# Kernel tuning notes

Measured on AMD Instinct MI355X. Metric: run time of the kernel, lower is better.

The kernel has to match this reference:

```python
import jax, jax.numpy as jnp
import numpy as np


def setup_inputs() -> dict:
    key = jax.random.key(0)
    ks = jax.random.split(key, 6)
    m, d, n, p = 4096, 1024, 16, 1024  # tokens, input_dim, num_experts, output_dim (=slots)
    h = (d + p) * 2 // 3  # 1365, hidden_dim per original module
    s = 0.02
    return {
        "x": jax.random.normal(ks[0], (m, d), jnp.float32),
        "phi": jax.random.normal(ks[1], (d, n, p), jnp.float32) * s,
        "W1": jax.random.normal(ks[2], (n, d, h), jnp.float32) * s,
        "b1": jax.random.normal(ks[3], (n, h), jnp.float32) * s,
        "W2": jax.random.normal(ks[4], (n, h, p), jnp.float32) * s,
        "b2": jax.random.normal(ks[5], (n, p), jnp.float32) * s,
    }


def reference(x, phi, W1, b1, W2, b2):
    # logits: [m, n, p] = tokens x experts x slots
    logits = jnp.einsum('md,dnp->mnp', x, phi)
    # Dispatch weights: softmax over tokens' expert axis (dim=1 in torch == experts n)
    D = jax.nn.softmax(logits, axis=1)
    # Combine weights: softmax over all (expert, slot) pairs per token
    m = logits.shape[0]
    C = jax.nn.softmax(logits.reshape(m, -1), axis=-1).reshape(logits.shape)
    # Slot inputs: [n, p, d]
    Xs = jnp.einsum('md,mnp->npd', x, D)
    # Batched per-expert MLP (replaces the Python loop over experts)
    H = jax.nn.relu(jnp.einsum('npd,ndh->nph', Xs, W1) + b1[:, None, :])
    Ys = jnp.einsum('nph,nho->npo', H, W2) + b2[:, None, :]  # [n, p, out]
    # Combine: [m, out]; flatten(start_dim=1) on a 2D tensor is a no-op
    Y = jnp.einsum('npo,mnp->mo', Ys, C)
    return Y
```

## Files before the change

### kernel.cpp

```cpp
#include <hip/hip_runtime.h>
#include <math.h>

#define MTOK 4096
#define DDIM 1024
#define NEXP 16
#define PSLOT 1024
#define NPDIM 16384
#define HDIM 1365
#define HPAD 1376
#define KSPL 4

typedef unsigned short u16;
typedef __attribute__((ext_vector_type(8))) short short8;
typedef __attribute__((ext_vector_type(8))) unsigned short ushort8;
typedef __attribute__((ext_vector_type(4))) unsigned int uint32x4;
typedef __attribute__((ext_vector_type(4))) float f32x4;

template<bool Bc, typename T, typename F> struct cond_t { using type = T; };
template<typename T, typename F> struct cond_t<false, T, F> { using type = F; };

__device__ __forceinline__ float b2f(u16 v) {
    union { unsigned int u; float f; } x;
    x.u = ((unsigned int)v) << 16;
    return x.f;
}
__device__ __forceinline__ u16 f2b(float f) {
    union { float f; unsigned int u; } x;
    x.f = f;
    unsigned int r = x.u + 0x7FFFu + ((x.u >> 16) & 1u);
    return (u16)(r >> 16);
}
__device__ __forceinline__ unsigned int cvtpk(float lo, float hi) {
    unsigned int r;
    asm("v_cvt_pk_bf16_f32 %0, %1, %2" : "=v"(r) : "v"(lo), "v"(hi));
    return r;
}
__device__ __forceinline__ void stv(float* p, long long i, float v) { p[i] = v; }
__device__ __forceinline__ void stv(u16*  p, long long i, float v) { p[i] = f2b(v); }

template<int AMODE, typename TA, typename TB, typename TC,
         bool BIASF, bool RELUF, bool ROWSC, bool BCHK>
__global__ __launch_bounds__(256) void mgemm(
    const TA* __restrict__ A, long long sA, int lda,
    const TB* __restrict__ B, long long sB, int ldb,
    TC* __restrict__ C, long long sC, int ldc,
    const float* __restrict__ S,
    const float* __restrict__ bias, long long sBias,
    const float* __restrict__ rowsc,
    int M, int N, int NZ, int K, int Kb, int Nb)
{
    constexpr int AS = (AMODE == 0) ? 32 : 40;
    constexpr int BS = 40;
    __shared__ u16 As[2][128 * AS];
    __shared__ u16 Bs[2][128 * BS];

    const int bz = blockIdx.z;
    A += (long long)bz * sA;
    B += (long long)bz * sB;
    C += (long long)bz * sC;
    const float* biasp = BIASF ? (bias + (long long)bz * sBias) : nullptr;

    const int gx = gridDim.x;
    const int nwg = gx * gridDim.y;
    int wg = blockIdx.x + gx * blockIdx.y;
    wg = (wg & 7) * (nwg >> 3) + (wg >> 3);
    const int m0 = (wg / gx) * 128;
    const int n0 = (wg % gx) * 128;

    const int tid  = threadIdx.x;
    const int lane = tid & 63;
    const int wv   = tid >> 6;
    const int wm   = wv & 1;
    const int wn   = wv >> 1;
    const int quad = lane >> 4;
    const int l16  = lane & 15;

    const int pp   = tid & 63;
    const int cl0  = 2 * pp;
    const int ng0  = n0 + cl0;

    auto aoff = [&](int row, int k8) {
        int o = row * AS + k8 * 8;
        if constexpr (AMODE != 0) o ^= ((row >> 3) & 3) << 3;
        return o;
    };
    auto boff = [&](int row, int k8) {
        return (row * BS + k8 * 8) ^ (((row >> 3) & 3) << 3);
    };

    f32x4 acc[4][4];
#pragma unroll
    for (int i = 0; i < 4; ++i)
#pragma unroll
        for (int j = 0; j < 4; ++j) acc[i][j] = (f32x4){0.f, 0.f, 0.f, 0.f};

    using BRAW = typename cond_t<sizeof(TB) == 2, unsigned int[8], float[16]>::type;

    auto LOADA = [&](int k0, int buf, unsigned int (&araw)[8], float2 (&sr)[8]) {
        if constexpr (AMODE == 0) {
#pragma unroll
            for (int q = 0; q < 2; ++q) {
                const u16* gp = A + (long long)(m0 + wv * 32 + q * 16 + (lane >> 2)) * lda
                                  + k0 + (lane & 3) * 8;
                u16* lp = &As[buf][(wv * 32 + q * 16) * 32];
                __builtin_amdgcn_global_load_lds(
                    (const __attribute__((address_space(1))) unsigned int*)gp,
                    (__attribute__((address_space(3))) unsigned int*)lp, 16, 0, 0);
            }
        } else {
#pragma unroll
            for (int i = 0; i < 8; ++i) {
                const long long kg = k0 + wv * 8 + i;
                araw[i] = *(const unsigned int*)((const u16*)A + kg * lda + (m0 + cl0));
                sr[i]   = *(const float2*)&S[kg * 1024 + ((m0 + cl0) & 1023)];
            }
        }
    };
    auto WRITEA = [&](int buf, unsigned int (&araw)[8], float2 (&sr)[8]) {
        if constexpr (AMODE != 0) {
            uint32x4 wa, wb;
#pragma unroll
            for (int j = 0; j < 4; ++j) {
                const unsigned int r0 = araw[2 * j], r1 = araw[2 * j + 1];
                wa[j] = cvtpk(b2f((u16)(r0 & 0xFFFFu)) * sr[2 * j].x,
                              b2f((u16)(r1 & 0xFFFFu)) * sr[2 * j + 1].x);
                wb[j] = cvtpk(b2f((u16)(r0 >> 16)) * sr[2 * j].y,
                              b2f((u16)(r1 >> 16)) * sr[2 * j + 1].y);
            }
            *(uint32x4*)&As[buf][aoff(cl0, wv)]     = wa;
            *(uint32x4*)&As[buf][aoff(cl0 + 1, wv)] = wb;
        }
    };
    auto LOADB = [&](int k0, BRAW& braw) {
        if constexpr (sizeof(TB) == 2) {
#pragma unroll
            for (int i = 0; i < 8; ++i) {
                const int kg = k0 + wv * 8 + i;
                braw[i] = *(const unsigned int*)((const u16*)B + (long long)kg * ldb + ng0);
            }
        } else {
            bool full = true;
            if constexpr (BCHK) full = (k0 + 32 <= Kb) && (n0 + 128 <= Nb);
            if (full) {
#pragma unroll
                for (int i = 0; i < 8; ++i) {
                    const int kg = k0 + wv * 8 + i;
                    const float* bp = (const float*)B + (long long)kg * ldb + ng0;
                    braw[2 * i]     = bp[0];
                    braw[2 * i + 1] = bp[1];
                }
            } else {
#pragma unroll
                for (int i = 0; i < 8; ++i) {
                    const int kg = k0 + wv * 8 + i;
                    float v0 = 0.f, v1 = 0.f;
                    if (kg < Kb) {
                        if (ng0 < Nb)     v0 = ((const float*)B)[(long long)kg * ldb + ng0];
                        if (ng0 + 1 < Nb) v1 = ((const float*)B)[(long long)kg * ldb + ng0 + 1];
                    }
                    braw[2 * i]     = v0;
                    braw[2 * i + 1] = v1;
                }
            }
        }
    };
    auto WRITEB = [&](int buf, BRAW& braw) {
        uint32x4 wa, wb;
        if constexpr (sizeof(TB) == 2) {
#pragma unroll
            for (int j = 0; j < 4; ++j) {
                const unsigned int r0 = braw[2 * j], r1 = braw[2 * j + 1];
                wa[j] = (r0 & 0xFFFFu) | (r1 << 16);
                wb[j] = (r0 >> 16) | (r1 & 0xFFFF0000u);
            }
        } else {
#pragma unroll
            for (int j = 0; j < 4; ++j) {
                wa[j] = cvtpk(braw[4 * j],     braw[4 * j + 2]);
                wb[j] = cvtpk(braw[4 * j + 1], braw[4 * j + 3]);
            }
        }
        *(uint32x4*)&Bs[buf][boff(cl0, wv)]     = wa;
        *(uint32x4*)&Bs[buf][boff(cl0 + 1, wv)] = wb;
    };
    auto MM = [&](int buf) {
        short8 bfr[4];
#pragma unroll
        for (int ni = 0; ni < 4; ++ni)
            bfr[ni] = *(const short8*)&Bs[buf][boff(wn * 64 + ni * 16 + l16, quad)];
#pragma unroll
        for (int mi = 0; mi < 4; ++mi) {
            short8 a = *(const short8*)&As[buf][aoff(wm * 64 + mi * 16 + l16, quad)];
#pragma unroll
            for (int ni = 0; ni < 4; ++ni)
                acc[mi][ni] = __builtin_amdgcn_mfma_f32_16x16x32_bf16(a, bfr[ni], acc[mi][ni], 0, 0, 0);
        }
    };

    const int nt = K >> 5;
    {
        unsigned int araw[8];
        float2 sr[8];
        BRAW braw;
        LOADA(0, 0, araw, sr);
        LOADB(0, braw);
        WRITEA(0, araw, sr);
        WRITEB(0, braw);
        __syncthreads();
    }
    for (int t = 0; t < nt; ++t) {
        const int cur = t & 1, nxt = cur ^ 1;
        unsigned int araw[8];
        float2 sr[8];
        BRAW braw;
        const bool pf = (t + 1 < nt);
        if (pf) {
            LOADA((t + 1) * 32, nxt, araw, sr);
            LOADB((t + 1) * 32, braw);
        }
        MM(cur);
        if (pf) {
            WRITEA(nxt, araw, sr);
            WRITEB(nxt, braw);
        }
        __syncthreads();
    }

#pragma unroll
    for (int mi = 0; mi < 4; ++mi) {
#pragma unroll
        for (int r = 0; r < 4; ++r) {
            const int rg = m0 + wm * 64 + mi * 16 + quad * 4 + r;
            if (rg >= M) continue;
            const float rs = ROWSC ? rowsc[rg] : 1.f;
#pragma unroll
            for (int ni = 0; ni < 4; ++ni) {
                const int cg = n0 + wn * 64 + ni * 16 + l16;
                if (cg < N) {
                    float v = acc[mi][ni][r];
                    if (BIASF) v += biasp[cg];
                    if (RELUF) v = fmaxf(v, 0.f);
                    if (ROWSC) v *= rs;
                    stv(C, (long long)rg * ldc + cg, v);
                } else if (cg < NZ) {
                    stv(C, (long long)rg * ldc + cg, 0.f);
                }
            }
        }
    }
}

__global__ __launch_bounds__(256) void cvt_k(
    const float* __restrict__ src, u16* __restrict__ dst, long long n)
{
    const long long i = ((long long)blockIdx.x * 256 + threadIdx.x) * 8;
    if (i >= n) return;
    const float4 a = *(const float4*)&src[i];
    const float4 b = *(const float4*)&src[i + 4];
    uint32x4 v;
    v[0] = cvtpk(a.x, a.y);
    v[1] = cvtpk(a.z, a.w);
    v[2] = cvtpk(b.x, b.y);
    v[3] = cvtpk(b.z, b.w);
    *(uint32x4*)&dst[i] = v;
}

__global__ __launch_bounds__(256) void softmax_k(
    u16* __restrict__ L, float* __restrict__ rsd, float* __restrict__ rsc)
{
    const int m = blockIdx.x;
    u16* row = L + (long long)m * NPDIM;
    const int tid = threadIdx.x;
    __shared__ float red[256];

    float mx = -1e30f;
    for (int i = tid * 8; i < NPDIM; i += 2048) {
        const ushort8 v = *(const ushort8*)&row[i];
#pragma unroll
        for (int j = 0; j < 8; ++j) mx = fmaxf(mx, b2f(v[j]));
    }
    red[tid] = mx;
    __syncthreads();
    for (int s = 128; s > 0; s >>= 1) {
        if (tid < s) red[tid] = fmaxf(red[tid], red[tid + s]);
        __syncthreads();
    }
    const float mxAll = red[0];
    __syncthreads();

    float sum = 0.f;
    for (int i = tid * 8; i < NPDIM; i += 2048) {
        const ushort8 v = *(const ushort8*)&row[i];
        ushort8 e;
#pragma unroll
        for (int j = 0; j < 8; ++j) {
            const float ef = __expf(b2f(v[j]) - mxAll);
            const u16 eb = f2b(ef);
            e[j] = eb;
            sum += b2f(eb);
        }
        *(ushort8*)&row[i] = e;
    }
    red[tid] = sum;
    __syncthreads();
    for (int s = 128; s > 0; s >>= 1) {
        if (tid < s) red[tid] += red[tid + s];
        __syncthreads();
    }
    if (tid == 0) rsc[m] = 1.f / red[0];
    __syncthreads();

    {
        const int p0 = tid * 4;
        float s0 = 0.f, s1 = 0.f, s2 = 0.f, s3 = 0.f;
#pragma unroll
        for (int n = 0; n < NEXP; ++n) {
            const ushort4 v = *(const ushort4*)&row[n * PSLOT + p0];
            s0 += b2f(v.x); s1 += b2f(v.y); s2 += b2f(v.z); s3 += b2f(v.w);
        }
        const float4 r = {1.f / s0, 1.f / s1, 1.f / s2, 1.f / s3};
        *(float4*)&rsd[(long long)m * PSLOT + p0] = r;
    }
}

__global__ __launch_bounds__(256) void reduce_k(
    const float* __restrict__ Yp, float* __restrict__ Y)
{
    const long long S = (long long)MTOK * PSLOT;
    const long long i = ((long long)blockIdx.x * 256 + threadIdx.x) * 4;
    f32x4 r = *(const f32x4*)&Yp[i];
#pragma unroll
    for (int z = 1; z < KSPL; ++z) r += *(const f32x4*)&Yp[(long long)z * S + i];
    *(f32x4*)&Y[i] = r;
}

extern "C" void kernel_launch(void* const* d_in, const int* in_sizes, int n_in,
                              void* d_out, int out_size, void* d_ws, size_t ws_size,
                              hipStream_t stream)
{
    const float* x   = (const float*)d_in[0];
    const float* phi = (const float*)d_in[1];
    const float* W1  = (const float*)d_in[2];
    const float* b1  = (const float*)d_in[3];
    const float* W2  = (const float*)d_in[4];
    const float* b2  = (const float*)d_in[5];
    float* Y = (float*)d_out;

    char* w = (char*)d_ws;
    u16*   L    = (u16*)w;   w += (size_t)MTOK * NPDIM * 2;
    u16*   Ys   = (u16*)w;   w += (size_t)NEXP * PSLOT * PSLOT * 2;
    float* rsc  = (float*)w; w += (size_t)MTOK * 4;
    float* Yp   = (float*)w;
    float* rsd  = (float*)w; w += (size_t)MTOK * PSLOT * 4;
    u16*   Xs   = (u16*)w;   w += (size_t)NEXP * PSLOT * DDIM * 2;
    u16*   Hb   = (u16*)w;   w += (size_t)NEXP * PSLOT * HPAD * 2;
    u16*   phib = Ys;
    u16*   xb   = Hb;

    cvt_k<<<dim3((MTOK * DDIM) / (8 * 256)), 256, 0, stream>>>(x, xb, (long long)MTOK * DDIM);
    cvt_k<<<dim3((DDIM * NPDIM) / (8 * 256)), 256, 0, stream>>>(phi, phib, (long long)DDIM * NPDIM);

    mgemm<0, u16, u16, u16, false, false, false, false>
        <<<dim3(NPDIM / 128, MTOK / 128, 1), 256, 0, stream>>>(
        xb, 0, DDIM,  phib, 0, NPDIM,  L, 0, NPDIM,
        nullptr, nullptr, 0, nullptr,
        MTOK, NPDIM, NPDIM, DDIM, DDIM, NPDIM);

    softmax_k<<<dim3(MTOK), 256, 0, stream>>>(L, rsd, rsc);

    mgemm<2, u16, u16, u16, false, false, false, false>
        <<<dim3(DDIM / 128, NPDIM / 128, 1), 256, 0, stream>>>(
        L, 0, NPDIM,  xb, 0, DDIM,  Xs, 0, DDIM,
        rsd, nullptr, 0, nullptr,
        NPDIM, DDIM, DDIM, MTOK, MTOK, DDIM);

    mgemm<0, u16, float, u16, true, true, false, true>
        <<<dim3((HPAD + 127) / 128, PSLOT / 128, NEXP), 256, 0, stream>>>(
        Xs, (long long)PSLOT * DDIM, DDIM,
        W1, (long long)DDIM * HDIM, HDIM,
        Hb, (long long)PSLOT * HPAD, HPAD,
        nullptr, b1, HDIM, nullptr,
        PSLOT, HDIM, HPAD, DDIM, DDIM, HDIM);

    mgemm<0, u16, float, u16, true, false, false, true>
        <<<dim3(PSLOT / 128, PSLOT / 128, NEXP), 256, 0, stream>>>(
        Hb, (long long)PSLOT * HPAD, HPAD,
        W2, (long long)HDIM * PSLOT, PSLOT,
        Ys, (long long)PSLOT * PSLOT, PSLOT,
        nullptr, b2, PSLOT, nullptr,
        PSLOT, PSLOT, PSLOT, HPAD, HDIM, PSLOT);

    mgemm<0, u16, u16, float, false, false, true, false>
        <<<dim3(PSLOT / 128, MTOK / 128, KSPL), 256, 0, stream>>>(
        L, (long long)(NPDIM / KSPL), NPDIM,
        Ys, (long long)(NPDIM / KSPL) * PSLOT, PSLOT,
        Yp, (long long)MTOK * PSLOT, PSLOT,
        nullptr, nullptr, 0, rsc,
        MTOK, PSLOT, PSLOT, NPDIM / KSPL, NPDIM / KSPL, PSLOT);

    reduce_k<<<dim3((MTOK * PSLOT) / (4 * 256)), 256, 0, stream>>>(Yp, Y);
}
```

Before: 1.347 ms.

## Enlarge GEMM tiles to 256x128 with 512-thread blocks

Grows the shared GEMM kernel's output tile from 128x128 to 256x128 by running 8 waves per block. The B tile is now staged once for twice as many rows, which halves B global loads and LDS writes per output. The grid swizzle is reworked to handle workgroup counts that are not a multiple of 8. The cost is more LDS per block, fewer blocks in the batched MLP GEMMs, and possibly lower occupancy.

```diff
diff --git a/kernel.cpp b/kernel.cpp
--- a/kernel.cpp
+++ b/kernel.cpp
@@ -13,6 +13,7 @@
 typedef unsigned short u16;
 typedef __attribute__((ext_vector_type(8))) short short8;
 typedef __attribute__((ext_vector_type(8))) unsigned short ushort8;
+typedef __attribute__((ext_vector_type(2))) unsigned int uint32x2;
 typedef __attribute__((ext_vector_type(4))) unsigned int uint32x4;
 typedef __attribute__((ext_vector_type(4))) float f32x4;
 
@@ -40,7 +41,7 @@
 
 template<int AMODE, typename TA, typename TB, typename TC,
          bool BIASF, bool RELUF, bool ROWSC, bool BCHK>
-__global__ __launch_bounds__(256) void mgemm(
+__global__ __launch_bounds__(512) void mgemm(
     const TA* __restrict__ A, long long sA, int lda,
     const TB* __restrict__ B, long long sB, int ldb,
     TC* __restrict__ C, long long sC, int ldc,
@@ -51,7 +52,7 @@
 {
     constexpr int AS = (AMODE == 0) ? 32 : 40;
     constexpr int BS = 40;
-    __shared__ u16 As[2][128 * AS];
+    __shared__ u16 As[2][256 * AS];
     __shared__ u16 Bs[2][128 * BS];
 
     const int bz = blockIdx.z;
@@ -63,29 +64,34 @@
     const int gx = gridDim.x;
     const int nwg = gx * gridDim.y;
     int wg = blockIdx.x + gx * blockIdx.y;
-    wg = (wg & 7) * (nwg >> 3) + (wg >> 3);
-    const int m0 = (wg / gx) * 128;
+    {
+        const int q = nwg >> 3, r = nwg & 7, xc = wg & 7, ix = wg >> 3;
+        wg = (xc < r ? xc * (q + 1) : r + xc * q) + ix;
+    }
+    const int m0 = (wg / gx) * 256;
     const int n0 = (wg % gx) * 128;
 
     const int tid  = threadIdx.x;
     const int lane = tid & 63;
     const int wv   = tid >> 6;
-    const int wm   = wv & 1;
-    const int wn   = wv >> 1;
+    const int wm   = wv & 3;
+    const int wn   = wv >> 2;
     const int quad = lane >> 4;
     const int l16  = lane & 15;
 
-    const int pp   = tid & 63;
-    const int cl0  = 2 * pp;
-    const int ng0  = n0 + cl0;
+    const int cla  = 2 * (tid & 127);
+    const int k8a  = tid >> 7;
+    const int clb  = 2 * (tid & 63);
+    const int kqb  = tid >> 6;
+    const int ngb  = n0 + clb;
 
     auto aoff = [&](int row, int k8) {
         int o = row * AS + k8 * 8;
         if constexpr (AMODE != 0) o ^= ((row >> 3) & 3) << 3;
         return o;
     };
-    auto boff = [&](int row, int k8) {
-        return (row * BS + k8 * 8) ^ (((row >> 3) & 3) << 3);
+    auto boff = [&](int row, int kel) {
+        return (row * BS + kel) ^ (((row >> 3) & 3) << 3);
     };
 
     f32x4 acc[4][4];
@@ -94,7 +100,7 @@
 #pragma unroll
         for (int j = 0; j < 4; ++j) acc[i][j] = (f32x4){0.f, 0.f, 0.f, 0.f};
 
-    using BRAW = typename cond_t<sizeof(TB) == 2, unsigned int[8], float[16]>::type;
+    using BRAW = typename cond_t<sizeof(TB) == 2, unsigned int[4], float[8]>::type;
 
     auto LOADA = [&](int k0, int buf, unsigned int (&araw)[8], float2 (&sr)[8]) {
         if constexpr (AMODE == 0) {
@@ -110,9 +116,9 @@
         } else {
 #pragma unroll
             for (int i = 0; i < 8; ++i) {
-                const long long kg = k0 + wv * 8 + i;
-                araw[i] = *(const unsigned int*)((const u16*)A + kg * lda + (m0 + cl0));
-                sr[i]   = *(const float2*)&S[kg * 1024 + ((m0 + cl0) & 1023)];
+                const long long kg = k0 + k8a * 8 + i;
+                araw[i] = *(const unsigned int*)((const u16*)A + kg * lda + (m0 + cla));
+                sr[i]   = *(const float2*)&S[kg * 1024 + ((m0 + cla) & 1023)];
             }
         }
     };
@@ -127,36 +133,36 @@
                 wb[j] = cvtpk(b2f((u16)(r0 >> 16)) * sr[2 * j].y,
                               b2f((u16)(r1 >> 16)) * sr[2 * j + 1].y);
             }
-            *(uint32x4*)&As[buf][aoff(cl0, wv)]     = wa;
-            *(uint32x4*)&As[buf][aoff(cl0 + 1, wv)] = wb;
+            *(uint32x4*)&As[buf][aoff(cla, k8a)]     = wa;
+            *(uint32x4*)&As[buf][aoff(cla + 1, k8a)] = wb;
         }
     };
     auto LOADB = [&](int k0, BRAW& braw) {
         if constexpr (sizeof(TB) == 2) {
 #pragma unroll
-            for (int i = 0; i < 8; ++i) {
-                const int kg = k0 + wv * 8 + i;
-                braw[i] = *(const unsigned int*)((const u16*)B + (long long)kg * ldb + ng0);
+            for (int i = 0; i < 4; ++i) {
+                const int kg = k0 + kqb * 4 + i;
+                braw[i] = *(const unsigned int*)((const u16*)B + (long long)kg * ldb + ngb);
             }
         } else {
             bool full = true;
             if constexpr (BCHK) full = (k0 + 32 <= Kb) && (n0 + 128 <= Nb);
             if (full) {
 #pragma unroll
-                for (int i = 0; i < 8; ++i) {
-                    const int kg = k0 + wv * 8 + i;
-                    const float* bp = (const float*)B + (long long)kg * ldb + ng0;
+                for (int i = 0; i < 4; ++i) {
+                    const int kg = k0 + kqb * 4 + i;
+                    const float* bp = (const float*)B + (long long)kg * ldb + ngb;
                     braw[2 * i]     = bp[0];
                     braw[2 * i + 1] = bp[1];
                 }
             } else {
 #pragma unroll
-                for (int i = 0; i < 8; ++i) {
-                    const int kg = k0 + wv * 8 + i;
+                for (int i = 0; i < 4; ++i) {
+                    const int kg = k0 + kqb * 4 + i;
                     float v0 = 0.f, v1 = 0.f;
                     if (kg < Kb) {
-                        if (ng0 < Nb)     v0 = ((const float*)B)[(long long)kg * ldb + ng0];
-                        if (ng0 + 1 < Nb) v1 = ((const float*)B)[(long long)kg * ldb + ng0 + 1];
+                        if (ngb < Nb)     v0 = ((const float*)B)[(long long)kg * ldb + ngb];
+                        if (ngb + 1 < Nb) v1 = ((const float*)B)[(long long)kg * ldb + ngb + 1];
                     }
                     braw[2 * i]     = v0;
                     braw[2 * i + 1] = v1;
@@ -165,29 +171,26 @@
         }
     };
     auto WRITEB = [&](int buf, BRAW& braw) {
-        uint32x4 wa, wb;
+        uint32x2 wa, wb;
         if constexpr (sizeof(TB) == 2) {
-#pragma unroll
-            for (int j = 0; j < 4; ++j) {
-                const unsigned int r0 = braw[2 * j], r1 = braw[2 * j + 1];
-                wa[j] = (r0 & 0xFFFFu) | (r1 << 16);
-                wb[j] = (r0 >> 16) | (r1 & 0xFFFF0000u);
-            }
+            wa[0] = (braw[0] & 0xFFFFu) | (braw[1] << 16);
+            wa[1] = (braw[2] & 0xFFFFu) | (braw[3] << 16);
+            wb[0] = (braw[0] >> 16) | (braw[1] & 0xFFFF0000u);
+            wb[1] = (braw[2] >> 16) | (braw[3] & 0xFFFF0000u);
         } else {
-#pragma unroll
-            for (int j = 0; j < 4; ++j) {
-                wa[j] = cvtpk(braw[4 * j],     braw[4 * j + 2]);
-                wb[j] = cvtpk(braw[4 * j + 1], braw[4 * j + 3]);
-            }
-        }
-        *(uint32x4*)&Bs[buf][boff(cl0, wv)]     = wa;
-        *(uint32x4*)&Bs[buf][boff(cl0 + 1, wv)] = wb;
+            wa[0] = cvtpk(braw[0], braw[2]);
+            wa[1] = cvtpk(braw[4], braw[6]);
+            wb[0] = cvtpk(braw[1], braw[3]);
+            wb[1] = cvtpk(braw[5], braw[7]);
+        }
+        *(uint32x2*)&Bs[buf][boff(clb, kqb * 4)]     = wa;
+        *(uint32x2*)&Bs[buf][boff(clb + 1, kqb * 4)] = wb;
     };
     auto MM = [&](int buf) {
         short8 bfr[4];
 #pragma unroll
         for (int ni = 0; ni < 4; ++ni)
-            bfr[ni] = *(const short8*)&Bs[buf][boff(wn * 64 + ni * 16 + l16, quad)];
+            bfr[ni] = *(const short8*)&Bs[buf][boff(wn * 64 + ni * 16 + l16, quad * 8)];
 #pragma unroll
         for (int mi = 0; mi < 4; ++mi) {
             short8 a = *(const short8*)&As[buf][aoff(wm * 64 + mi * 16 + l16, quad)];
@@ -361,7 +364,7 @@
     cvt_k<<<dim3((DDIM * NPDIM) / (8 * 256)), 256, 0, stream>>>(phi, phib, (long long)DDIM * NPDIM);
 
     mgemm<0, u16, u16, u16, false, false, false, false>
-        <<<dim3(NPDIM / 128, MTOK / 128, 1), 256, 0, stream>>>(
+        <<<dim3(NPDIM / 128, MTOK / 256, 1), 512, 0, stream>>>(
         xb, 0, DDIM,  phib, 0, NPDIM,  L, 0, NPDIM,
         nullptr, nullptr, 0, nullptr,
         MTOK, NPDIM, NPDIM, DDIM, DDIM, NPDIM);
@@ -369,13 +372,13 @@
     softmax_k<<<dim3(MTOK), 256, 0, stream>>>(L, rsd, rsc);
 
     mgemm<2, u16, u16, u16, false, false, false, false>
-        <<<dim3(DDIM / 128, NPDIM / 128, 1), 256, 0, stream>>>(
+        <<<dim3(DDIM / 128, NPDIM / 256, 1), 512, 0, stream>>>(
         L, 0, NPDIM,  xb, 0, DDIM,  Xs, 0, DDIM,
         rsd, nullptr, 0, nullptr,
         NPDIM, DDIM, DDIM, MTOK, MTOK, DDIM);
 
     mgemm<0, u16, float, u16, true, true, false, true>
-        <<<dim3((HPAD + 127) / 128, PSLOT / 128, NEXP), 256, 0, stream>>>(
+        <<<dim3((HPAD + 127) / 128, PSLOT / 256, NEXP), 512, 0, stream>>>(
         Xs, (long long)PSLOT * DDIM, DDIM,
         W1, (long long)DDIM * HDIM, HDIM,
         Hb, (long long)PSLOT * HPAD, HPAD,
@@ -383,7 +386,7 @@
         PSLOT, HDIM, HPAD, DDIM, DDIM, HDIM);
 
     mgemm<0, u16, float, u16, true, false, false, true>
-        <<<dim3(PSLOT / 128, PSLOT / 128, NEXP), 256, 0, stream>>>(
+        <<<dim3(PSLOT / 128, PSLOT / 256, NEXP), 512, 0, stream>>>(
         Hb, (long long)PSLOT * HPAD, HPAD,
         W2, (long long)HDIM * PSLOT, PSLOT,
         Ys, (long long)PSLOT * PSLOT, PSLOT,
@@ -391,7 +394,7 @@
         PSLOT, PSLOT, PSLOT, HPAD, HDIM, PSLOT);
 
     mgemm<0, u16, u16, float, false, false, true, false>
-        <<<dim3(PSLOT / 128, MTOK / 128, KSPL), 256, 0, stream>>>(
+        <<<dim3(PSLOT / 128, MTOK / 256, KSPL), 512, 0, stream>>>(
         L, (long long)(NPDIM / KSPL), NPDIM,
         Ys, (long long)(NPDIM / KSPL) * PSLOT, PSLOT,
         Yp, (long long)MTOK * PSLOT, PSLOT,
```

New measurement: 1.163 ms. 13.6% less time.
